# Kernel optimization log

Measured on AMD Instinct MI355X. Metric: run time of the kernel, lower is better.

Reference implementation:

```python
import jax, jax.numpy as jnp
import numpy as np

N, L, D, F, NUM_BAGS = 262144, 1024, 128, 32, 256


def setup_inputs() -> dict:
    key = jax.random.key(0)
    ks = jax.random.split(key, 12)
    x = jax.random.normal(ks[0], (N, L), dtype=jnp.float32)
    idxs = jnp.sort(jax.random.randint(ks[1], (N,), 0, NUM_BAGS, dtype=jnp.int64))
    def lin(k, fan_in, fan_out):
        s = 1.0 / np.sqrt(fan_in)
        return jax.random.uniform(k, (fan_in, fan_out), jnp.float32, -s, s)
    W1 = lin(ks[2], L, D);  b1 = jnp.zeros((D,), jnp.float32)
    Wt = lin(ks[3], D, F);  bt = jnp.zeros((F,), jnp.float32)
    Ws = lin(ks[4], D, F);  bs = jnp.zeros((F,), jnp.float32)
    Wa = lin(ks[5], F, 1);  ba = jnp.zeros((1,), jnp.float32)
    Wp = lin(ks[6], D, F);  bp = jnp.zeros((F,), jnp.float32)
    return {"x": x, "idxs": idxs, "W1": W1, "b1": b1, "Wt": Wt, "bt": bt,
            "Ws": Ws, "bs": bs, "Wa": Wa, "ba": ba, "Wp": Wp, "bp": bp}


def reference(x, idxs, W1, b1, Wt, bt, Ws, bs, Wa, ba, Wp, bp):
    # feature extractor (Dropout is identity at eval time)
    H = jax.nn.relu(x @ W1 + b1)                       # [N, D]
    # gated attention scores
    At = jnp.tanh(H @ Wt + bt)                         # [N, F]
    As = jax.nn.sigmoid(H @ Ws + bs)                   # [N, F]
    a = ((At * As) @ Wa + ba)[:, 0]                    # [N]
    # per-bag (segment) softmax, numerically stable
    amax = jax.ops.segment_max(a, idxs, num_segments=NUM_BAGS)   # [B]
    w = jnp.exp(a - amax[idxs])                         # [N]
    den = jax.ops.segment_sum(w, idxs, num_segments=NUM_BAGS)    # [B]
    w = w / den[idxs]
    # segment weighted reduce: M[b] = sum_i w_i * H_i over bag b
    M = jax.ops.segment_sum(w[:, None] * H, idxs, num_segments=NUM_BAGS)  # [B, D]
    # projector + L2 normalize (torch F.normalize eps=1e-12)
    proj = M @ Wp + bp                                  # [B, F]
    nrm = jnp.maximum(jnp.linalg.norm(proj, axis=1, keepdims=True), 1e-12)
    proj = proj / nrm
    return M, proj
```

## Files before the change

kernel.cpp:

```cpp
#include <hip/hip_runtime.h>
#include <hip/hip_bf16.h>

#define NTOT 262144
#define LDIM 1024
#define DDIM 128
#define FDIM 32
#define NBAGS 256

typedef __attribute__((ext_vector_type(8))) short bf16x8;
typedef __attribute__((ext_vector_type(4))) float f32x4;

__device__ __forceinline__ unsigned short f2b(float f) {
    __hip_bfloat16 h = __float2bfloat16(f);
    return __builtin_bit_cast(unsigned short, h);
}
__device__ __forceinline__ float b2f(unsigned short u) {
    union { float f; unsigned int i; } c;
    c.i = ((unsigned int)u) << 16;
    return c.f;
}

__global__ void k_prep(const float* __restrict__ W1, const int* __restrict__ idxs,
                       ushort* __restrict__ w1t2, int* __restrict__ bag_start) {
    int gid = blockIdx.x * 256 + threadIdx.x;
    if (gid < LDIM * DDIM) {
        int col = gid & 127, k = gid >> 7;
        int kt = k >> 6, ko = k & 63;
        int cc = ko >> 3, kr = ko & 7;
        int ccs = cc ^ (col & 7);
        w1t2[kt * 8192 + col * 64 + ccs * 8 + kr] = f2b(W1[gid]);
    }
    if (gid < NTOT) {
        int v = idxs[gid];
        int p = (gid == 0) ? -1 : idxs[gid - 1];
        for (int b = p + 1; b <= v; ++b) bag_start[b] = gid;
        if (gid == NTOT - 1)
            for (int b = v + 1; b <= NBAGS; ++b) bag_start[b] = NTOT;
    }
}

__global__ __launch_bounds__(256, 3) void k_fused_gemm(
    const float* __restrict__ x, const ushort* __restrict__ w1t2,
    const float* __restrict__ b1,
    const float* __restrict__ Wt, const float* __restrict__ bt,
    const float* __restrict__ Ws, const float* __restrict__ bs,
    const float* __restrict__ Wa, const float* __restrict__ ba,
    ushort* __restrict__ Hb, float* __restrict__ aout)
{
    __shared__ __align__(16) ushort sAB[16384];
    __shared__ __align__(16) ushort sWtT[4096];
    __shared__ __align__(16) ushort sWsT[4096];
    __shared__ float sb1[128];
    __shared__ float sbt[32], sbs[32], sWa[32];

    const int t    = threadIdx.x;
    const int lane = t & 63;
    const int wave = t >> 6;
    const int wr   = wave >> 1, wc = wave & 1;
    const int lq   = lane >> 4, lr = lane & 15;
    const int row0 = blockIdx.x * 128;

    for (int e = t; e < 4096; e += 256) {
        int d = e >> 5, f = e & 31;
        int byt = f * 256 + ((((d >> 3) ^ (f & 15))) << 4) + (d & 7) * 2;
        *(ushort*)((char*)sWtT + byt) = f2b(Wt[e]);
        *(ushort*)((char*)sWsT + byt) = f2b(Ws[e]);
    }
    if (t < 128) sb1[t] = b1[t];
    if (t < 32)  { sbt[t] = bt[t]; sbs[t] = bs[t]; sWa[t] = Wa[t]; }
    const float ba0 = ba[0];

    f32x4 acc[4][4];
#pragma unroll
    for (int m = 0; m < 4; ++m)
#pragma unroll
        for (int n = 0; n < 4; ++n) acc[m][n] = 0;

    char* sA = (char*)sAB;
    char* sB = (char*)sAB + 16384;

    const int arow  = t >> 4;
    const int acol4 = (t & 15) * 4;
    const float* xb = x + (size_t)(row0 + arow) * LDIM + acol4;
    const int a_base = (((acol4 >> 3) ^ (arow & 7)) << 4) + (acol4 & 7) * 2;
    const ushort* bb = w1t2 + t * 8;
    char* sBw = sB + t * 16;

    float4 av[8];
    bf16x8 bv[4];
#pragma unroll
    for (int j = 0; j < 8; ++j) av[j] = *(const float4*)(xb + j * (16 * LDIM));
#pragma unroll
    for (int jj = 0; jj < 4; ++jj) bv[jj] = *(const bf16x8*)(bb + jj * 2048);

    for (int kt = 0; kt < 16; ++kt) {
        __syncthreads();

#pragma unroll
        for (int j = 0; j < 8; ++j) {
            float4 f = av[j];
            uint2 pk;
            pk.x = (unsigned)f2b(f.x) | ((unsigned)f2b(f.y) << 16);
            pk.y = (unsigned)f2b(f.z) | ((unsigned)f2b(f.w) << 16);
            *(uint2*)(sA + (arow + 16 * j) * 128 + a_base) = pk;
        }
#pragma unroll
        for (int jj = 0; jj < 4; ++jj)
            *(bf16x8*)(sBw + jj * 4096) = bv[jj];
        __syncthreads();

        if (kt < 15) {
            const float* xk = xb + (kt + 1) * 64;
#pragma unroll
            for (int j = 0; j < 8; ++j) av[j] = *(const float4*)(xk + j * (16 * LDIM));
            const ushort* bk = bb + (kt + 1) * 8192;
#pragma unroll
            for (int jj = 0; jj < 4; ++jj) bv[jj] = *(const bf16x8*)(bk + jj * 2048);
        }

#pragma unroll
        for (int kk = 0; kk < 2; ++kk) {
            bf16x8 aF[4], bF[4];
#pragma unroll
            for (int m = 0; m < 4; ++m) {
                int ra = wr * 64 + m * 16 + lr;
                aF[m] = *(const bf16x8*)(sA + ra * 128 + (((kk * 4 + lq) ^ (ra & 7)) << 4));
            }
#pragma unroll
            for (int n = 0; n < 4; ++n) {
                int cb = wc * 64 + n * 16 + lr;
                bF[n] = *(const bf16x8*)(sB + cb * 128 + (((kk * 4 + lq) ^ (cb & 7)) << 4));
            }
#pragma unroll
            for (int m = 0; m < 4; ++m)
#pragma unroll
                for (int n = 0; n < 4; ++n)
                    acc[m][n] = __builtin_amdgcn_mfma_f32_16x16x32_bf16(aF[m], bF[n], acc[m][n], 0, 0, 0);
        }
    }
    __syncthreads();

    char* sH = (char*)sAB;
#pragma unroll
    for (int m = 0; m < 4; ++m) {
#pragma unroll
        for (int n = 0; n < 4; ++n) {
            const int colg = wc * 64 + n * 16 + lr;
            const float bias = sb1[colg];
#pragma unroll
            for (int r = 0; r < 4; ++r) {
                const int rowl = wr * 64 + m * 16 + lq * 4 + r;
                float h = acc[m][n][r] + bias;
                h = fmaxf(h, 0.0f);
                *(ushort*)(sH + rowl * 256 + (((colg >> 3) ^ (rowl & 15)) << 4) + (colg & 7) * 2) = f2b(h);
            }
        }
    }
    __syncthreads();

    ushort* Hg = Hb + (size_t)row0 * 128;
#pragma unroll
    for (int p = 0; p < 8; ++p) {
        int idx = p * 256 + t;
        int row = idx >> 4, slot = idx & 15;
        bf16x8 v = *(const bf16x8*)(sH + row * 256 + ((slot ^ (row & 15)) << 4));
        *(bf16x8*)(Hg + (size_t)row * 128 + slot * 8) = v;
    }

    {
        f32x4 at_[2][2], as_[2][2];
#pragma unroll
        for (int m = 0; m < 2; ++m)
#pragma unroll
            for (int n = 0; n < 2; ++n) { at_[m][n] = 0; as_[m][n] = 0; }

        const char* cWtT = (const char*)sWtT;
        const char* cWsT = (const char*)sWsT;
#pragma unroll
        for (int kk = 0; kk < 4; ++kk) {
            bf16x8 aH[2], bT[2], bS[2];
            const int slot = kk * 4 + lq;
#pragma unroll
            for (int m = 0; m < 2; ++m) {
                const int ra = wave * 32 + m * 16 + lr;
                aH[m] = *(const bf16x8*)(sH + ra * 256 + ((slot ^ (ra & 15)) << 4));
            }
#pragma unroll
            for (int n = 0; n < 2; ++n) {
                const int f = n * 16 + lr;
                bT[n] = *(const bf16x8*)(cWtT + f * 256 + ((slot ^ (f & 15)) << 4));
                bS[n] = *(const bf16x8*)(cWsT + f * 256 + ((slot ^ (f & 15)) << 4));
            }
#pragma unroll
            for (int m = 0; m < 2; ++m)
#pragma unroll
                for (int n = 0; n < 2; ++n) {
                    at_[m][n] = __builtin_amdgcn_mfma_f32_16x16x32_bf16(aH[m], bT[n], at_[m][n], 0, 0, 0);
                    as_[m][n] = __builtin_amdgcn_mfma_f32_16x16x32_bf16(aH[m], bS[n], as_[m][n], 0, 0, 0);
                }
        }

#pragma unroll
        for (int m = 0; m < 2; ++m) {
#pragma unroll
            for (int r = 0; r < 4; ++r) {
                float s = 0.f;
#pragma unroll
                for (int n = 0; n < 2; ++n) {
                    const int f = n * 16 + lr;
                    float tv = tanhf(at_[m][n][r] + sbt[f]);
                    float sg = 1.0f / (1.0f + __expf(-(as_[m][n][r] + sbs[f])));
                    s += tv * sg * sWa[f];
                }
                s += __shfl_xor(s, 1);
                s += __shfl_xor(s, 2);
                s += __shfl_xor(s, 4);
                s += __shfl_xor(s, 8);
                if (lr == 0)
                    aout[row0 + wave * 32 + m * 16 + lq * 4 + r] = s + ba0;
            }
        }
    }
}

__global__ __launch_bounds__(1024) void k_bag(
    const int* __restrict__ bag_start, const float* __restrict__ a,
    const ushort* __restrict__ Hb, const float* __restrict__ Wp,
    const float* __restrict__ bp, float* __restrict__ out)
{
    __shared__ float red[64 * 132];
    __shared__ float swv[16];
    __shared__ float sM[128];
    __shared__ float sbc[2];

    const int b = blockIdx.x, t = threadIdx.x;
    const int lane = t & 63, wave = t >> 6;

    const int start = bag_start[b];
    const int end   = bag_start[b + 1];

    float mx = -3.0e38f;
    for (int i = start + t; i < end; i += 1024) mx = fmaxf(mx, a[i]);
#pragma unroll
    for (int m = 1; m < 64; m <<= 1) mx = fmaxf(mx, __shfl_xor(mx, m));
    if (lane == 0) swv[wave] = mx;
    __syncthreads();
    if (t == 0) {
        float v = swv[0];
#pragma unroll
        for (int i = 1; i < 16; ++i) v = fmaxf(v, swv[i]);
        sbc[0] = v;
    }
    __syncthreads();
    const float amax = sbc[0];

    float sm = 0.f;
    for (int i = start + t; i < end; i += 1024) sm += __expf(a[i] - amax);
#pragma unroll
    for (int m = 1; m < 64; m <<= 1) sm += __shfl_xor(sm, m);
    if (lane == 0) swv[wave] = sm;
    __syncthreads();
    if (t == 0) {
        float v = 0.f;
#pragma unroll
        for (int i = 0; i < 16; ++i) v += swv[i];
        sbc[1] = v;
    }
    __syncthreads();
    const float den = sbc[1];
    const float inv_den = den > 0.f ? 1.0f / den : 0.0f;

    const int cg = t & 15, rg = t >> 4;
    float acc[8];
#pragma unroll
    for (int j = 0; j < 8; ++j) acc[j] = 0.f;
    for (int i = start + rg; i < end; i += 64) {
        float w = __expf(a[i] - amax);
        bf16x8 h = *(const bf16x8*)(Hb + (size_t)i * 128 + cg * 8);
#pragma unroll
        for (int j = 0; j < 8; ++j) acc[j] += w * b2f((unsigned short)h[j]);
    }
#pragma unroll
    for (int j = 0; j < 8; ++j) red[rg * 132 + cg * 8 + j] = acc[j];
    __syncthreads();

    if (t < 128) {
        float s = 0.f;
        for (int r = 0; r < 64; ++r) s += red[r * 132 + t];
        s *= inv_den;
        sM[t] = s;
        out[b * 128 + t] = s;
    }
    __syncthreads();

    if (t < 32) {
        float p = bp[t];
        for (int d = 0; d < 128; ++d) p += sM[d] * Wp[d * 32 + t];
        float ss = p * p;
#pragma unroll
        for (int m = 1; m < 32; m <<= 1) ss += __shfl_xor(ss, m);
        float nrm = sqrtf(ss);
        out[32768 + b * 32 + t] = p / fmaxf(nrm, 1e-12f);
    }
}

extern "C" void kernel_launch(void* const* d_in, const int* in_sizes, int n_in,
                              void* d_out, int out_size, void* d_ws, size_t ws_size,
                              hipStream_t stream)
{
    const float* x  = (const float*)d_in[0];
    const int*   idxs = (const int*)d_in[1];
    const float* W1 = (const float*)d_in[2];
    const float* b1 = (const float*)d_in[3];
    const float* Wt = (const float*)d_in[4];
    const float* bt = (const float*)d_in[5];
    const float* Ws = (const float*)d_in[6];
    const float* bs = (const float*)d_in[7];
    const float* Wa = (const float*)d_in[8];
    const float* ba = (const float*)d_in[9];
    const float* Wp = (const float*)d_in[10];
    const float* bp = (const float*)d_in[11];
    float* out = (float*)d_out;

    char* ws = (char*)d_ws;
    ushort* Hb   = (ushort*)ws;
    ushort* w1t2 = (ushort*)(ws + 67108864);
    float*  aN   = (float*) (ws + 67108864 + 262144);
    int*    bagS = (int*)   (ws + 67108864 + 262144 + 1048576);

    k_prep<<<1024, 256, 0, stream>>>(W1, idxs, w1t2, bagS);
    k_fused_gemm<<<2048, 256, 0, stream>>>(x, w1t2, b1, Wt, bt, Ws, bs, Wa, ba, Hb, aN);
    k_bag<<<NBAGS, 1024, 0, stream>>>(bagS, aN, Hb, Wp, bp, out);
}
```

Measured before the change: 265.9 us.

## Fuse segment-weighted bag reduction into GEMM epilogue with atomic accumulation

The per-bag weighted sum of H and the softmax denominator are now computed in the GEMM kernel's epilogue. Each block accumulates exp(a)*H runs per bag from shared memory and flushes them with global atomics. This removes the bf16 H write and re-read, the separate score buffer and the bag_start scan, and the final kernel only normalises and projects. In exchange it drops the per-bag max subtraction, relying on scores staying small enough for exp not to overflow. It also makes the float summation order depend on atomic ordering.

```diff
diff --git a/kernel.cpp b/kernel.cpp
--- a/kernel.cpp
+++ b/kernel.cpp
@@ -20,8 +20,8 @@
     return c.f;
 }
 
-__global__ void k_prep(const float* __restrict__ W1, const int* __restrict__ idxs,
-                       ushort* __restrict__ w1t2, int* __restrict__ bag_start) {
+__global__ void k_prep(const float* __restrict__ W1, ushort* __restrict__ w1t2,
+                       float* __restrict__ Mraw, float* __restrict__ dden) {
     int gid = blockIdx.x * 256 + threadIdx.x;
     if (gid < LDIM * DDIM) {
         int col = gid & 127, k = gid >> 7;
@@ -30,13 +30,8 @@
         int ccs = cc ^ (col & 7);
         w1t2[kt * 8192 + col * 64 + ccs * 8 + kr] = f2b(W1[gid]);
     }
-    if (gid < NTOT) {
-        int v = idxs[gid];
-        int p = (gid == 0) ? -1 : idxs[gid - 1];
-        for (int b = p + 1; b <= v; ++b) bag_start[b] = gid;
-        if (gid == NTOT - 1)
-            for (int b = v + 1; b <= NBAGS; ++b) bag_start[b] = NTOT;
-    }
+    if (gid < NBAGS * DDIM) Mraw[gid] = 0.0f;
+    if (gid < NBAGS) dden[gid] = 0.0f;
 }
 
 __global__ __launch_bounds__(256, 3) void k_fused_gemm(
@@ -45,13 +40,16 @@
     const float* __restrict__ Wt, const float* __restrict__ bt,
     const float* __restrict__ Ws, const float* __restrict__ bs,
     const float* __restrict__ Wa, const float* __restrict__ ba,
-    ushort* __restrict__ Hb, float* __restrict__ aout)
+    const int* __restrict__ idxs,
+    float* __restrict__ Mraw, float* __restrict__ dden)
 {
     __shared__ __align__(16) ushort sAB[16384];
     __shared__ __align__(16) ushort sWtT[4096];
     __shared__ __align__(16) ushort sWsT[4096];
     __shared__ float sb1[128];
     __shared__ float sbt[32], sbs[32], sWa[32];
+    __shared__ float sw[128];
+    __shared__ int   sbag[128];
 
     const int t    = threadIdx.x;
     const int lane = t & 63;
@@ -66,7 +64,7 @@
         *(ushort*)((char*)sWtT + byt) = f2b(Wt[e]);
         *(ushort*)((char*)sWsT + byt) = f2b(Ws[e]);
     }
-    if (t < 128) sb1[t] = b1[t];
+    if (t < 128) { sb1[t] = b1[t]; sbag[t] = idxs[row0 + t]; }
     if (t < 32)  { sbt[t] = bt[t]; sbs[t] = bs[t]; sWa[t] = Wa[t]; }
     const float ba0 = ba[0];
 
@@ -157,15 +155,6 @@
         }
     }
     __syncthreads();
-
-    ushort* Hg = Hb + (size_t)row0 * 128;
-#pragma unroll
-    for (int p = 0; p < 8; ++p) {
-        int idx = p * 256 + t;
-        int row = idx >> 4, slot = idx & 15;
-        bf16x8 v = *(const bf16x8*)(sH + row * 256 + ((slot ^ (row & 15)) << 4));
-        *(bf16x8*)(Hg + (size_t)row * 128 + slot * 8) = v;
-    }
 
     {
         f32x4 at_[2][2], as_[2][2];
@@ -217,80 +206,48 @@
                 s += __shfl_xor(s, 4);
                 s += __shfl_xor(s, 8);
                 if (lr == 0)
-                    aout[row0 + wave * 32 + m * 16 + lq * 4 + r] = s + ba0;
-            }
-        }
-    }
-}
-
-__global__ __launch_bounds__(1024) void k_bag(
-    const int* __restrict__ bag_start, const float* __restrict__ a,
-    const ushort* __restrict__ Hb, const float* __restrict__ Wp,
-    const float* __restrict__ bp, float* __restrict__ out)
+                    sw[wave * 32 + m * 16 + lq * 4 + r] = __expf(s + ba0);
+            }
+        }
+    }
+    __syncthreads();
+
+    {
+        const int d = t & 127, half = t >> 7;
+        const int r0 = half * 64;
+        float accv = 0.f, accw = 0.f;
+        int curbag = sbag[r0];
+        for (int r = 0; r < 64; ++r) {
+            const int rr = r0 + r;
+            const int bg = sbag[rr];
+            if (bg != curbag) {
+                atomicAdd(&Mraw[curbag * 128 + d], accv);
+                if (d == 0) atomicAdd(&dden[curbag], accw);
+                accv = 0.f; accw = 0.f; curbag = bg;
+            }
+            const float w = sw[rr];
+            const ushort hv = *(const ushort*)(sH + rr * 256 + ((((d >> 3) ^ (rr & 15))) << 4) + (d & 7) * 2);
+            accv += w * b2f(hv);
+            accw += w;
+        }
+        atomicAdd(&Mraw[curbag * 128 + d], accv);
+        if (d == 0) atomicAdd(&dden[curbag], accw);
+    }
+}
+
+__global__ __launch_bounds__(128) void k_final(
+    const float* __restrict__ Mraw, const float* __restrict__ dden,
+    const float* __restrict__ Wp, const float* __restrict__ bp,
+    float* __restrict__ out)
 {
-    __shared__ float red[64 * 132];
-    __shared__ float swv[16];
     __shared__ float sM[128];
-    __shared__ float sbc[2];
-
     const int b = blockIdx.x, t = threadIdx.x;
-    const int lane = t & 63, wave = t >> 6;
-
-    const int start = bag_start[b];
-    const int end   = bag_start[b + 1];
-
-    float mx = -3.0e38f;
-    for (int i = start + t; i < end; i += 1024) mx = fmaxf(mx, a[i]);
-#pragma unroll
-    for (int m = 1; m < 64; m <<= 1) mx = fmaxf(mx, __shfl_xor(mx, m));
-    if (lane == 0) swv[wave] = mx;
-    __syncthreads();
-    if (t == 0) {
-        float v = swv[0];
-#pragma unroll
-        for (int i = 1; i < 16; ++i) v = fmaxf(v, swv[i]);
-        sbc[0] = v;
-    }
-    __syncthreads();
-    const float amax = sbc[0];
-
-    float sm = 0.f;
-    for (int i = start + t; i < end; i += 1024) sm += __expf(a[i] - amax);
-#pragma unroll
-    for (int m = 1; m < 64; m <<= 1) sm += __shfl_xor(sm, m);
-    if (lane == 0) swv[wave] = sm;
-    __syncthreads();
-    if (t == 0) {
-        float v = 0.f;
-#pragma unroll
-        for (int i = 0; i < 16; ++i) v += swv[i];
-        sbc[1] = v;
-    }
-    __syncthreads();
-    const float den = sbc[1];
+    const float den = dden[b];
     const float inv_den = den > 0.f ? 1.0f / den : 0.0f;
 
-    const int cg = t & 15, rg = t >> 4;
-    float acc[8];
-#pragma unroll
-    for (int j = 0; j < 8; ++j) acc[j] = 0.f;
-    for (int i = start + rg; i < end; i += 64) {
-        float w = __expf(a[i] - amax);
-        bf16x8 h = *(const bf16x8*)(Hb + (size_t)i * 128 + cg * 8);
-#pragma unroll
-        for (int j = 0; j < 8; ++j) acc[j] += w * b2f((unsigned short)h[j]);
-    }
-#pragma unroll
-    for (int j = 0; j < 8; ++j) red[rg * 132 + cg * 8 + j] = acc[j];
-    __syncthreads();
-
-    if (t < 128) {
-        float s = 0.f;
-        for (int r = 0; r < 64; ++r) s += red[r * 132 + t];
-        s *= inv_den;
-        sM[t] = s;
-        out[b * 128 + t] = s;
-    }
+    float m = Mraw[b * 128 + t] * inv_den;
+    sM[t] = m;
+    out[b * 128 + t] = m;
     __syncthreads();
 
     if (t < 32) {
@@ -298,7 +255,7 @@
         for (int d = 0; d < 128; ++d) p += sM[d] * Wp[d * 32 + t];
         float ss = p * p;
 #pragma unroll
-        for (int m = 1; m < 32; m <<= 1) ss += __shfl_xor(ss, m);
+        for (int mm = 1; mm < 32; mm <<= 1) ss += __shfl_xor(ss, mm);
         float nrm = sqrtf(ss);
         out[32768 + b * 32 + t] = p / fmaxf(nrm, 1e-12f);
     }
@@ -323,12 +280,11 @@
     float* out = (float*)d_out;
 
     char* ws = (char*)d_ws;
-    ushort* Hb   = (ushort*)ws;
-    ushort* w1t2 = (ushort*)(ws + 67108864);
-    float*  aN   = (float*) (ws + 67108864 + 262144);
-    int*    bagS = (int*)   (ws + 67108864 + 262144 + 1048576);
-
-    k_prep<<<1024, 256, 0, stream>>>(W1, idxs, w1t2, bagS);
-    k_fused_gemm<<<2048, 256, 0, stream>>>(x, w1t2, b1, Wt, bt, Ws, bs, Wa, ba, Hb, aN);
-    k_bag<<<NBAGS, 1024, 0, stream>>>(bagS, aN, Hb, Wp, bp, out);
-}
+    float*  Mraw = (float*)ws;
+    float*  dden = (float*)(ws + 131072);
+    ushort* w1t2 = (ushort*)(ws + 132096);
+
+    k_prep<<<512, 256, 0, stream>>>(W1, w1t2, Mraw, dden);
+    k_fused_gemm<<<2048, 256, 0, stream>>>(x, w1t2, b1, Wt, bt, Ws, bs, Wa, ba, idxs, Mraw, dden);
+    k_final<<<NBAGS, 128, 0, stream>>>(Mraw, dden, Wp, bp, out);
+}
```

After: 231.8 us. -12.8%, faster.
